# Performance work log

Hardware: AMD Instinct MI355X
Metric: run time of the kernel (lower is better)

Reference implementation:

```python
import jax, jax.numpy as jnp
import numpy as np

DIM = 512
HEADS = 8
DIM_HEAD = 64
INNER = HEADS * DIM_HEAD
SCALE = DIM_HEAD ** -0.5


def setup_inputs() -> dict:
    key = jax.random.key(0)
    ks = jax.random.split(key, 7)
    B, N = 8, 1024
    x = jax.random.normal(ks[0], (B, N, DIM), dtype=jnp.float32)
    rel_pos_bias = jax.random.normal(ks[1], (HEADS, N, N), dtype=jnp.float32) * 0.02
    w_qkv = jax.random.normal(ks[2], (DIM, 3 * INNER), dtype=jnp.float32) * (DIM ** -0.5)
    w_out = jax.random.normal(ks[3], (INNER, DIM), dtype=jnp.float32) * (INNER ** -0.5)
    b_out = jnp.zeros((DIM,), dtype=jnp.float32)
    ln_gamma = jnp.ones((DIM,), dtype=jnp.float32)
    ln_beta = jnp.zeros((DIM,), dtype=jnp.float32)
    return {"x": x, "rel_pos_bias": rel_pos_bias, "w_qkv": w_qkv,
            "w_out": w_out, "b_out": b_out, "ln_gamma": ln_gamma, "ln_beta": ln_beta}


def _layernorm(x, gamma, beta, eps=1e-5):
    mu = jnp.mean(x, axis=-1, keepdims=True)
    var = jnp.var(x, axis=-1, keepdims=True)
    return (x - mu) * jax.lax.rsqrt(var + eps) * gamma + beta


def reference(x, rel_pos_bias, w_qkv, w_out, b_out, ln_gamma, ln_beta):
    B, N, _ = x.shape
    xn = _layernorm(x, ln_gamma, ln_beta)
    qkv = xn @ w_qkv  # [B,N,3*INNER]
    q, k, v = jnp.split(qkv, 3, axis=-1)
    # b n (h d) -> b h n d
    reshape = lambda t: t.reshape(B, N, HEADS, DIM_HEAD).transpose(0, 2, 1, 3)
    q, k, v = reshape(q) * SCALE, reshape(k), reshape(v)
    sim = jnp.einsum('bhid,bhjd->bhij', q, k)
    sim = sim + rel_pos_bias  # broadcast [h,N,N] over batch
    attn = jax.nn.softmax(sim, axis=-1)
    out = jnp.einsum('bhij,bhjd->bhid', attn, v)
    out = out.transpose(0, 2, 1, 3).reshape(B, N, INNER)
    return out @ w_out + b_out
```

## Files before the change

kernel.cpp:

```cpp
#include <hip/hip_runtime.h>
#include <hip/hip_bf16.h>

#define DIM 512
#define HEADS 8
#define DHEAD 64
#define INNER 512
#define NSEQ 1024
#define BATCH 8
#define MROWS (BATCH*NSEQ)
#define QK_SCALE 0.125f

typedef __attribute__((ext_vector_type(4))) float f32x4;
typedef __attribute__((ext_vector_type(8))) short short8;
typedef unsigned short ushort_t;

__device__ inline ushort_t f2bf(float f) {
    __hip_bfloat16 h = __float2bfloat16(f);
    return *reinterpret_cast<ushort_t*>(&h);
}
__device__ inline float bf2f(ushort_t u) {
    union { unsigned int i; float f; } c; c.i = ((unsigned int)u) << 16; return c.f;
}

__global__ __launch_bounds__(256) void ln_kernel(const float* __restrict__ x,
        const float* __restrict__ gamma, const float* __restrict__ beta,
        ushort_t* __restrict__ xn) {
    int row = blockIdx.x * 4 + (threadIdx.x >> 6);
    int lane = threadIdx.x & 63;
    const float4* xr = (const float4*)(x + (size_t)row * DIM);
    float4 a0 = xr[lane];
    float4 a1 = xr[lane + 64];
    float s  = a0.x + a0.y + a0.z + a0.w + a1.x + a1.y + a1.z + a1.w;
    float ss = a0.x*a0.x + a0.y*a0.y + a0.z*a0.z + a0.w*a0.w
             + a1.x*a1.x + a1.y*a1.y + a1.z*a1.z + a1.w*a1.w;
    for (int off = 1; off < 64; off <<= 1) {
        s  += __shfl_xor(s, off);
        ss += __shfl_xor(ss, off);
    }
    float mean = s * (1.0f / DIM);
    float var  = ss * (1.0f / DIM) - mean * mean;
    float inv  = rsqrtf(var + 1e-5f);
    const float4* g4 = (const float4*)gamma;
    const float4* b4 = (const float4*)beta;
    float4 g0 = g4[lane], g1 = g4[lane + 64];
    float4 be0 = b4[lane], be1 = b4[lane + 64];
    ushort4 o0, o1;
    o0.x = f2bf((a0.x - mean) * inv * g0.x + be0.x);
    o0.y = f2bf((a0.y - mean) * inv * g0.y + be0.y);
    o0.z = f2bf((a0.z - mean) * inv * g0.z + be0.z);
    o0.w = f2bf((a0.w - mean) * inv * g0.w + be0.w);
    o1.x = f2bf((a1.x - mean) * inv * g1.x + be1.x);
    o1.y = f2bf((a1.y - mean) * inv * g1.y + be1.y);
    o1.z = f2bf((a1.z - mean) * inv * g1.z + be1.z);
    o1.w = f2bf((a1.w - mean) * inv * g1.w + be1.w);
    ushort4* outr = (ushort4*)(xn + (size_t)row * DIM);
    outr[lane] = o0;
    outr[lane + 64] = o1;
}

__global__ __launch_bounds__(256) void transpose_cast(const float* __restrict__ w,
        ushort_t* __restrict__ wt, int ncols) {
    __shared__ ushort_t T[64][72];
    int n0 = blockIdx.x * 64, k0 = blockIdx.y * 64;
    int t = threadIdx.x;
    int kr = t >> 2;
    int nc = (t & 3) * 16;
    const float4* src = (const float4*)(w + (size_t)(k0 + kr) * ncols + n0 + nc);
    float4 f0 = src[0], f1 = src[1], f2 = src[2], f3 = src[3];
    ushort_t tmp[16];
    tmp[0]=f2bf(f0.x); tmp[1]=f2bf(f0.y); tmp[2]=f2bf(f0.z); tmp[3]=f2bf(f0.w);
    tmp[4]=f2bf(f1.x); tmp[5]=f2bf(f1.y); tmp[6]=f2bf(f1.z); tmp[7]=f2bf(f1.w);
    tmp[8]=f2bf(f2.x); tmp[9]=f2bf(f2.y); tmp[10]=f2bf(f2.z); tmp[11]=f2bf(f2.w);
    tmp[12]=f2bf(f3.x); tmp[13]=f2bf(f3.y); tmp[14]=f2bf(f3.z); tmp[15]=f2bf(f3.w);
    *(uint4*)&T[kr][nc]     = *(uint4*)&tmp[0];
    *(uint4*)&T[kr][nc + 8] = *(uint4*)&tmp[8];
    __syncthreads();
    int nr = t >> 2;
    int kc = (t & 3) * 16;
    ushort_t o[16];
    for (int j = 0; j < 16; j++) o[j] = T[kc + j][nr];
    ushort_t* dst = wt + (size_t)(n0 + nr) * 512 + k0 + kc;
    *(uint4*)(dst)     = *(uint4*)&o[0];
    *(uint4*)(dst + 8) = *(uint4*)&o[8];
}

__global__ __launch_bounds__(256) void bias_cvt(const float* __restrict__ in,
        ushort_t* __restrict__ out) {
    int i = blockIdx.x * 256 + threadIdx.x;
    float4 v = ((const float4*)in)[i];
    ushort4 o;
    o.x = f2bf(v.x); o.y = f2bf(v.y); o.z = f2bf(v.z); o.w = f2bf(v.w);
    ((ushort4*)out)[i] = o;
}

__global__ __launch_bounds__(256) void v_transpose(const ushort_t* __restrict__ vb,
        ushort_t* __restrict__ vt) {
    __shared__ ushort_t T[64][72];
    int bh = blockIdx.y;
    int s0 = blockIdx.x * 64;
    int t = threadIdx.x;
    int row = t >> 2, c = (t & 3) * 16;
    const ushort_t* src = vb + ((size_t)bh * NSEQ + s0 + row) * DHEAD + c;
    *(uint4*)&T[row][c]     = *(const uint4*)(src);
    *(uint4*)&T[row][c + 8] = *(const uint4*)(src + 8);
    __syncthreads();
    int d = t >> 2;
    int sq = (t & 3) * 16;
    ushort_t tmp[16];
    for (int j = 0; j < 16; j++) tmp[j] = T[sq + j][d];
    *(uint4*)(vt + ((size_t)bh * DHEAD + d) * NSEQ + s0 + sq)     = *(uint4*)&tmp[0];
    *(uint4*)(vt + ((size_t)bh * DHEAD + d) * NSEQ + s0 + sq + 8) = *(uint4*)&tmp[8];
}

template<int EPI>
__global__ __launch_bounds__(256) void gemm_kernel(
        const ushort_t* __restrict__ A, const ushort_t* __restrict__ Bt,
        ushort_t* __restrict__ qb, ushort_t* __restrict__ kb, ushort_t* __restrict__ vb,
        float* __restrict__ outp, const float* __restrict__ bvec) {
    __shared__ ushort_t Als[128][72];
    __shared__ ushort_t Bls[128][72];
    int t = threadIdx.x;
    int bm = blockIdx.y, bn = blockIdx.x;
    int lane = t & 63, w = t >> 6, wm = w >> 1, wn = w & 1;
    int l15 = lane & 15, l4 = lane >> 4;
    f32x4 acc[4][4] = {};
    int srow = t >> 1;
    int sc   = (t & 1) * 32;

    for (int kt = 0; kt < DIM / 64; ++kt) {
        __syncthreads();
        {
            const ushort_t* ap = A  + (size_t)(bm*128 + srow) * DIM + kt*64 + sc;
            const ushort_t* bp = Bt + (size_t)(bn*128 + srow) * DIM + kt*64 + sc;
            uint4 a0 = *(const uint4*)(ap);
            uint4 a1 = *(const uint4*)(ap + 8);
            uint4 a2 = *(const uint4*)(ap + 16);
            uint4 a3 = *(const uint4*)(ap + 24);
            uint4 b0 = *(const uint4*)(bp);
            uint4 b1 = *(const uint4*)(bp + 8);
            uint4 b2 = *(const uint4*)(bp + 16);
            uint4 b3 = *(const uint4*)(bp + 24);
            *(uint4*)&Als[srow][sc]      = a0;
            *(uint4*)&Als[srow][sc + 8]  = a1;
            *(uint4*)&Als[srow][sc + 16] = a2;
            *(uint4*)&Als[srow][sc + 24] = a3;
            *(uint4*)&Bls[srow][sc]      = b0;
            *(uint4*)&Bls[srow][sc + 8]  = b1;
            *(uint4*)&Bls[srow][sc + 16] = b2;
            *(uint4*)&Bls[srow][sc + 24] = b3;
        }
        __syncthreads();
        for (int ks = 0; ks < 2; ks++) {
            short8 af[4], bfr[4];
            for (int mi = 0; mi < 4; mi++) af[mi]  = *(const short8*)&Als[wm*64 + mi*16 + l15][ks*32 + l4*8];
            for (int ni = 0; ni < 4; ni++) bfr[ni] = *(const short8*)&Bls[wn*64 + ni*16 + l15][ks*32 + l4*8];
            __builtin_amdgcn_s_setprio(1);
            for (int mi = 0; mi < 4; mi++)
                for (int ni = 0; ni < 4; ni++)
                    acc[mi][ni] = __builtin_amdgcn_mfma_f32_16x16x32_bf16(bfr[ni], af[mi], acc[mi][ni], 0, 0, 0);
            __builtin_amdgcn_s_setprio(0);
        }
    }

    for (int mi = 0; mi < 4; mi++) {
        int r = bm*128 + wm*64 + mi*16 + l15;
        for (int ni = 0; ni < 4; ni++) {
            int c = bn*128 + wn*64 + ni*16 + l4*4;
            f32x4 v = acc[mi][ni];
            if (EPI == 0) {
                int part = c >> 9, cw = c & 511;
                int h = cw >> 6, d = cw & 63;
                int b = r >> 10, i = r & 1023;
                size_t off = (((size_t)(b*HEADS + h)) * NSEQ + i) * DHEAD + d;
                ushort4 o;
                if (part == 0) {
                    o.x = f2bf(v[0] * QK_SCALE); o.y = f2bf(v[1] * QK_SCALE);
                    o.z = f2bf(v[2] * QK_SCALE); o.w = f2bf(v[3] * QK_SCALE);
                    *(ushort4*)(qb + off) = o;
                } else if (part == 1) {
                    o.x = f2bf(v[0]); o.y = f2bf(v[1]); o.z = f2bf(v[2]); o.w = f2bf(v[3]);
                    *(ushort4*)(kb + off) = o;
                } else {
                    o.x = f2bf(v[0]); o.y = f2bf(v[1]); o.z = f2bf(v[2]); o.w = f2bf(v[3]);
                    *(ushort4*)(vb + off) = o;
                }
            } else {
                float4 bv = *(const float4*)(bvec + c);
                float4 o2;
                o2.x = v[0] + bv.x; o2.y = v[1] + bv.y;
                o2.z = v[2] + bv.z; o2.w = v[3] + bv.w;
                *(float4*)(outp + (size_t)r * DIM + c) = o2;
            }
        }
    }
}

__global__ __launch_bounds__(256) void attn_kernel(
        const ushort_t* __restrict__ q, const ushort_t* __restrict__ k,
        const ushort_t* __restrict__ vt, const ushort_t* __restrict__ biasb,
        ushort_t* __restrict__ attno) {
    __shared__ ushort_t Kls[64][72];
    __shared__ ushort_t Vtls[64][72];
    __shared__ ushort_t Pls[4][16][72];
    int t = threadIdx.x, lane = t & 63, w = t >> 6;
    int l15 = lane & 15, l4 = lane >> 4;
    int b = blockIdx.z, h = blockIdx.y, q0 = blockIdx.x * 64;
    size_t bh = (size_t)(b * HEADS + h);
    const ushort_t* qp = q  + (bh * NSEQ + q0 + w*16) * DHEAD;
    const ushort_t* kp = k  + bh * NSEQ * DHEAD;
    const ushort_t* vp = vt + bh * DHEAD * NSEQ;
    int qrow = q0 + w*16 + l15;
    const ushort_t* bp = biasb + ((size_t)h * NSEQ + qrow) * NSEQ;

    short8 bq[2];
    bq[0] = *(const short8*)(qp + l15*DHEAD + l4*8);
    bq[1] = *(const short8*)(qp + l15*DHEAD + l4*8 + 32);

    f32x4 o[4] = {};
    float mrun = -INFINITY, lrun = 0.f;

    int srow = t >> 2, sc = (t & 3) * 16;

    uint4 kreg0, kreg1, vreg0, vreg1;
    {
        const ushort_t* ks0 = kp + (size_t)srow * DHEAD + sc;
        const ushort_t* vs0 = vp + (size_t)srow * NSEQ + sc;
        kreg0 = *(const uint4*)(ks0);
        kreg1 = *(const uint4*)(ks0 + 8);
        vreg0 = *(const uint4*)(vs0);
        vreg1 = *(const uint4*)(vs0 + 8);
    }

    for (int kt = 0; kt < NSEQ / 64; ++kt) {
        __syncthreads();
        *(uint4*)&Kls[srow][sc]      = kreg0;
        *(uint4*)&Kls[srow][sc + 8]  = kreg1;
        *(uint4*)&Vtls[srow][sc]     = vreg0;
        *(uint4*)&Vtls[srow][sc + 8] = vreg1;
        __syncthreads();

        if (kt + 1 < NSEQ / 64) {
            const ushort_t* ksn = kp + (size_t)((kt+1)*64 + srow) * DHEAD + sc;
            const ushort_t* vsn = vp + (size_t)srow * NSEQ + (kt+1)*64 + sc;
            kreg0 = *(const uint4*)(ksn);
            kreg1 = *(const uint4*)(ksn + 8);
            vreg0 = *(const uint4*)(vsn);
            vreg1 = *(const uint4*)(vsn + 8);
        }

        f32x4 s[4];
        __builtin_amdgcn_s_setprio(1);
        for (int ni = 0; ni < 4; ni++) {
            f32x4 z = {};
            short8 ak0 = *(const short8*)&Kls[ni*16 + l15][l4*8];
            short8 ak1 = *(const short8*)&Kls[ni*16 + l15][l4*8 + 32];
            z = __builtin_amdgcn_mfma_f32_16x16x32_bf16(ak0, bq[0], z, 0, 0, 0);
            z = __builtin_amdgcn_mfma_f32_16x16x32_bf16(ak1, bq[1], z, 0, 0, 0);
            s[ni] = z;
        }
        __builtin_amdgcn_s_setprio(0);

        float p[16];
        float mj = -INFINITY;
        for (int ni = 0; ni < 4; ni++) {
            ushort4 b4 = *(const ushort4*)(bp + kt*64 + ni*16 + l4*4);
            float v0 = s[ni][0] + bf2f(b4.x);
            float v1 = s[ni][1] + bf2f(b4.y);
            float v2 = s[ni][2] + bf2f(b4.z);
            float v3 = s[ni][3] + bf2f(b4.w);
            p[ni*4+0] = v0; p[ni*4+1] = v1; p[ni*4+2] = v2; p[ni*4+3] = v3;
            mj = fmaxf(mj, fmaxf(fmaxf(v0, v1), fmaxf(v2, v3)));
        }
        mj = fmaxf(mj, __shfl_xor(mj, 16));
        mj = fmaxf(mj, __shfl_xor(mj, 32));
        if (!__all(mj <= mrun + 8.f)) {
            float mnew = fmaxf(mrun, mj);
            float scl = __expf(mrun - mnew);
            lrun *= scl;
            for (int di = 0; di < 4; di++) o[di] *= scl;
            mrun = mnew;
        }
        float rs = 0.f;
        for (int i = 0; i < 16; i++) {
            p[i] = __expf(p[i] - mrun);
            rs += p[i];
        }
        rs += __shfl_xor(rs, 16);
        rs += __shfl_xor(rs, 32);
        lrun += rs;

        for (int ni = 0; ni < 4; ni++) {
            ushort4 pk;
            pk.x = f2bf(p[ni*4+0]); pk.y = f2bf(p[ni*4+1]);
            pk.z = f2bf(p[ni*4+2]); pk.w = f2bf(p[ni*4+3]);
            *(ushort4*)&Pls[w][l15][ni*16 + l4*4] = pk;
        }

        __builtin_amdgcn_s_setprio(1);
        for (int ks2 = 0; ks2 < 2; ks2++) {
            short8 pb = *(const short8*)&Pls[w][l15][ks2*32 + l4*8];
            for (int di = 0; di < 4; di++) {
                short8 av = *(const short8*)&Vtls[di*16 + l15][ks2*32 + l4*8];
                o[di] = __builtin_amdgcn_mfma_f32_16x16x32_bf16(av, pb, o[di], 0, 0, 0);
            }
        }
        __builtin_amdgcn_s_setprio(0);
    }

    float inv = 1.0f / lrun;
    for (int di = 0; di < 4; di++) {
        ushort4 ov;
        ov.x = f2bf(o[di][0] * inv);
        ov.y = f2bf(o[di][1] * inv);
        ov.z = f2bf(o[di][2] * inv);
        ov.w = f2bf(o[di][3] * inv);
        *(ushort4*)(attno + ((size_t)(b*NSEQ + qrow)) * INNER + h*DHEAD + di*16 + l4*4) = ov;
    }
}

extern "C" void kernel_launch(void* const* d_in, const int* in_sizes, int n_in,
                              void* d_out, int out_size, void* d_ws, size_t ws_size,
                              hipStream_t stream) {
    (void)in_sizes; (void)n_in; (void)out_size; (void)ws_size;
    const float* x      = (const float*)d_in[0];
    const float* bias   = (const float*)d_in[1];
    const float* w_qkv  = (const float*)d_in[2];
    const float* w_out  = (const float*)d_in[3];
    const float* b_out  = (const float*)d_in[4];
    const float* gamma  = (const float*)d_in[5];
    const float* beta   = (const float*)d_in[6];
    float* out = (float*)d_out;

    ushort_t* xn    = (ushort_t*)d_ws;
    ushort_t* wqkvT = xn + (size_t)MROWS * DIM;
    ushort_t* woutT = wqkvT + (size_t)1536 * 512;
    ushort_t* qb    = woutT + (size_t)512 * 512;
    ushort_t* kb    = qb + (size_t)MROWS * INNER;
    ushort_t* vb    = kb + (size_t)MROWS * INNER;
    ushort_t* vt    = vb + (size_t)MROWS * INNER;
    ushort_t* attn  = vt + (size_t)MROWS * INNER;
    ushort_t* biasb = attn + (size_t)MROWS * INNER;

    hipLaunchKernelGGL(ln_kernel, dim3(MROWS / 4), dim3(256), 0, stream, x, gamma, beta, xn);
    hipLaunchKernelGGL(transpose_cast, dim3(1536 / 64, 512 / 64), dim3(256), 0, stream, w_qkv, wqkvT, 3 * INNER);
    hipLaunchKernelGGL(transpose_cast, dim3(512 / 64, 512 / 64), dim3(256), 0, stream, w_out, woutT, DIM);
    hipLaunchKernelGGL(bias_cvt, dim3(HEADS * NSEQ * NSEQ / 4 / 256), dim3(256), 0, stream, bias, biasb);
    hipLaunchKernelGGL((gemm_kernel<0>), dim3(1536 / 128, MROWS / 128), dim3(256), 0, stream,
                       xn, wqkvT, qb, kb, vb, nullptr, nullptr);
    hipLaunchKernelGGL(v_transpose, dim3(NSEQ / 64, BATCH * HEADS), dim3(256), 0, stream, vb, vt);
    hipLaunchKernelGGL(attn_kernel, dim3(NSEQ / 64, HEADS, BATCH), dim3(256), 0, stream,
                       qb, kb, vt, biasb, attn);
    hipLaunchKernelGGL((gemm_kernel<1>), dim3(DIM / 128, MROWS / 128), dim3(256), 0, stream,
                       attn, woutT, nullptr, nullptr, nullptr, out, b_out);
}
```

Measured before the change: 203.8 us.

## Fuse prep kernels, write V transposed, prefetch GEMM tiles, use exp2 softmax

Merges layernorm, both weight transpose-casts and the bias conversion into one prep kernel. The QKV GEMM epilogue now writes V directly in transposed layout, which removes the separate v_transpose kernel. Both GEMMs gain register prefetch of the next K tile, and the output GEMM uses a 64-wide N tile so more blocks launch. In the attention kernel, log2e is folded into Q and the bias so the softmax can use raw v_exp_f32, and the next bias tile is prefetched into registers. The transposed V stores are scalar and strided, which may cost write efficiency.

```diff
diff --git a/kernel.cpp b/kernel.cpp
--- a/kernel.cpp
+++ b/kernel.cpp
@@ -9,6 +9,7 @@
 #define BATCH 8
 #define MROWS (BATCH*NSEQ)
 #define QK_SCALE 0.125f
+#define LOG2E 1.44269504f
 
 typedef __attribute__((ext_vector_type(4))) float f32x4;
 typedef __attribute__((ext_vector_type(8))) short short8;
@@ -21,48 +22,12 @@
 __device__ inline float bf2f(ushort_t u) {
     union { unsigned int i; float f; } c; c.i = ((unsigned int)u) << 16; return c.f;
 }
-
-__global__ __launch_bounds__(256) void ln_kernel(const float* __restrict__ x,
-        const float* __restrict__ gamma, const float* __restrict__ beta,
-        ushort_t* __restrict__ xn) {
-    int row = blockIdx.x * 4 + (threadIdx.x >> 6);
-    int lane = threadIdx.x & 63;
-    const float4* xr = (const float4*)(x + (size_t)row * DIM);
-    float4 a0 = xr[lane];
-    float4 a1 = xr[lane + 64];
-    float s  = a0.x + a0.y + a0.z + a0.w + a1.x + a1.y + a1.z + a1.w;
-    float ss = a0.x*a0.x + a0.y*a0.y + a0.z*a0.z + a0.w*a0.w
-             + a1.x*a1.x + a1.y*a1.y + a1.z*a1.z + a1.w*a1.w;
-    for (int off = 1; off < 64; off <<= 1) {
-        s  += __shfl_xor(s, off);
-        ss += __shfl_xor(ss, off);
-    }
-    float mean = s * (1.0f / DIM);
-    float var  = ss * (1.0f / DIM) - mean * mean;
-    float inv  = rsqrtf(var + 1e-5f);
-    const float4* g4 = (const float4*)gamma;
-    const float4* b4 = (const float4*)beta;
-    float4 g0 = g4[lane], g1 = g4[lane + 64];
-    float4 be0 = b4[lane], be1 = b4[lane + 64];
-    ushort4 o0, o1;
-    o0.x = f2bf((a0.x - mean) * inv * g0.x + be0.x);
-    o0.y = f2bf((a0.y - mean) * inv * g0.y + be0.y);
-    o0.z = f2bf((a0.z - mean) * inv * g0.z + be0.z);
-    o0.w = f2bf((a0.w - mean) * inv * g0.w + be0.w);
-    o1.x = f2bf((a1.x - mean) * inv * g1.x + be1.x);
-    o1.y = f2bf((a1.y - mean) * inv * g1.y + be1.y);
-    o1.z = f2bf((a1.z - mean) * inv * g1.z + be1.z);
-    o1.w = f2bf((a1.w - mean) * inv * g1.w + be1.w);
-    ushort4* outr = (ushort4*)(xn + (size_t)row * DIM);
-    outr[lane] = o0;
-    outr[lane + 64] = o1;
-}
-
-__global__ __launch_bounds__(256) void transpose_cast(const float* __restrict__ w,
-        ushort_t* __restrict__ wt, int ncols) {
-    __shared__ ushort_t T[64][72];
-    int n0 = blockIdx.x * 64, k0 = blockIdx.y * 64;
-    int t = threadIdx.x;
+__device__ inline float fast_exp2(float x) {
+    float r; asm("v_exp_f32 %0, %1" : "=v"(r) : "v"(x)); return r;
+}
+
+__device__ inline void tc_tile(const float* __restrict__ w, ushort_t* __restrict__ wt,
+        int ncols, int n0, int k0, int t, ushort_t (*T)[72]) {
     int kr = t >> 2;
     int nc = (t & 3) * 16;
     const float4* src = (const float4*)(w + (size_t)(k0 + kr) * ncols + n0 + nc);
@@ -84,79 +49,109 @@
     *(uint4*)(dst + 8) = *(uint4*)&o[8];
 }
 
-__global__ __launch_bounds__(256) void bias_cvt(const float* __restrict__ in,
-        ushort_t* __restrict__ out) {
-    int i = blockIdx.x * 256 + threadIdx.x;
-    float4 v = ((const float4*)in)[i];
-    ushort4 o;
-    o.x = f2bf(v.x); o.y = f2bf(v.y); o.z = f2bf(v.z); o.w = f2bf(v.w);
-    ((ushort4*)out)[i] = o;
-}
-
-__global__ __launch_bounds__(256) void v_transpose(const ushort_t* __restrict__ vb,
-        ushort_t* __restrict__ vt) {
+__global__ __launch_bounds__(256) void prep_kernel(
+        const float* __restrict__ x, const float* __restrict__ gamma,
+        const float* __restrict__ beta, ushort_t* __restrict__ xn,
+        const float* __restrict__ w_qkv, ushort_t* __restrict__ wqkvT,
+        const float* __restrict__ w_out, ushort_t* __restrict__ woutT,
+        const float* __restrict__ bias, ushort_t* __restrict__ biasb) {
     __shared__ ushort_t T[64][72];
-    int bh = blockIdx.y;
-    int s0 = blockIdx.x * 64;
+    int bid = blockIdx.x;
     int t = threadIdx.x;
-    int row = t >> 2, c = (t & 3) * 16;
-    const ushort_t* src = vb + ((size_t)bh * NSEQ + s0 + row) * DHEAD + c;
-    *(uint4*)&T[row][c]     = *(const uint4*)(src);
-    *(uint4*)&T[row][c + 8] = *(const uint4*)(src + 8);
-    __syncthreads();
-    int d = t >> 2;
-    int sq = (t & 3) * 16;
-    ushort_t tmp[16];
-    for (int j = 0; j < 16; j++) tmp[j] = T[sq + j][d];
-    *(uint4*)(vt + ((size_t)bh * DHEAD + d) * NSEQ + s0 + sq)     = *(uint4*)&tmp[0];
-    *(uint4*)(vt + ((size_t)bh * DHEAD + d) * NSEQ + s0 + sq + 8) = *(uint4*)&tmp[8];
-}
-
-template<int EPI>
+    if (bid < 2048) {
+        int row = bid * 4 + (t >> 6);
+        int lane = t & 63;
+        const float4* xr = (const float4*)(x + (size_t)row * DIM);
+        float4 a0 = xr[lane];
+        float4 a1 = xr[lane + 64];
+        float s  = a0.x + a0.y + a0.z + a0.w + a1.x + a1.y + a1.z + a1.w;
+        float ss = a0.x*a0.x + a0.y*a0.y + a0.z*a0.z + a0.w*a0.w
+                 + a1.x*a1.x + a1.y*a1.y + a1.z*a1.z + a1.w*a1.w;
+        for (int off = 1; off < 64; off <<= 1) {
+            s  += __shfl_xor(s, off);
+            ss += __shfl_xor(ss, off);
+        }
+        float mean = s * (1.0f / DIM);
+        float var  = ss * (1.0f / DIM) - mean * mean;
+        float inv  = rsqrtf(var + 1e-5f);
+        const float4* g4 = (const float4*)gamma;
+        const float4* b4 = (const float4*)beta;
+        float4 g0 = g4[lane], g1 = g4[lane + 64];
+        float4 be0 = b4[lane], be1 = b4[lane + 64];
+        ushort4 o0, o1;
+        o0.x = f2bf((a0.x - mean) * inv * g0.x + be0.x);
+        o0.y = f2bf((a0.y - mean) * inv * g0.y + be0.y);
+        o0.z = f2bf((a0.z - mean) * inv * g0.z + be0.z);
+        o0.w = f2bf((a0.w - mean) * inv * g0.w + be0.w);
+        o1.x = f2bf((a1.x - mean) * inv * g1.x + be1.x);
+        o1.y = f2bf((a1.y - mean) * inv * g1.y + be1.y);
+        o1.z = f2bf((a1.z - mean) * inv * g1.z + be1.z);
+        o1.w = f2bf((a1.w - mean) * inv * g1.w + be1.w);
+        ushort4* outr = (ushort4*)(xn + (size_t)row * DIM);
+        outr[lane] = o0;
+        outr[lane + 64] = o1;
+    } else if (bid < 2240) {
+        int rel = bid - 2048;
+        tc_tile(w_qkv, wqkvT, 1536, (rel % 24) * 64, (rel / 24) * 64, t, T);
+    } else if (bid < 2304) {
+        int rel = bid - 2240;
+        tc_tile(w_out, woutT, 512, (rel % 8) * 64, (rel / 8) * 64, t, T);
+    } else {
+        int rel = bid - 2304;
+        int i = rel * 256 + t;
+        float4 v = ((const float4*)bias)[i];
+        ushort4 o;
+        o.x = f2bf(v.x * LOG2E); o.y = f2bf(v.y * LOG2E);
+        o.z = f2bf(v.z * LOG2E); o.w = f2bf(v.w * LOG2E);
+        ((ushort4*)biasb)[i] = o;
+    }
+}
+
+template<int EPI, int BN>
 __global__ __launch_bounds__(256) void gemm_kernel(
         const ushort_t* __restrict__ A, const ushort_t* __restrict__ Bt,
-        ushort_t* __restrict__ qb, ushort_t* __restrict__ kb, ushort_t* __restrict__ vb,
+        ushort_t* __restrict__ qb, ushort_t* __restrict__ kb, ushort_t* __restrict__ vtb,
         float* __restrict__ outp, const float* __restrict__ bvec) {
+    constexpr int BNF = BN / 32;
     __shared__ ushort_t Als[128][72];
-    __shared__ ushort_t Bls[128][72];
+    __shared__ ushort_t Bls[BN][72];
     int t = threadIdx.x;
     int bm = blockIdx.y, bn = blockIdx.x;
     int lane = t & 63, w = t >> 6, wm = w >> 1, wn = w & 1;
     int l15 = lane & 15, l4 = lane >> 4;
-    f32x4 acc[4][4] = {};
-    int srow = t >> 1;
-    int sc   = (t & 1) * 32;
+    f32x4 acc[4][BNF] = {};
+
+    int ra = t >> 1, ca = (t & 1) * 32;
+    int rb, cb_;
+    if constexpr (BN == 128) { rb = t >> 1; cb_ = (t & 1) * 32; }
+    else                     { rb = t >> 2; cb_ = (t & 3) * 16; }
+
+    uint4 ar[4], br[BN == 128 ? 4 : 2];
+    {
+        const ushort_t* ap = A  + (size_t)(bm*128 + ra) * DIM + ca;
+        for (int i = 0; i < 4; i++) ar[i] = *(const uint4*)(ap + i*8);
+        const ushort_t* bp = Bt + (size_t)(bn*BN + rb) * DIM + cb_;
+        for (int i = 0; i < (BN == 128 ? 4 : 2); i++) br[i] = *(const uint4*)(bp + i*8);
+    }
 
     for (int kt = 0; kt < DIM / 64; ++kt) {
         __syncthreads();
-        {
-            const ushort_t* ap = A  + (size_t)(bm*128 + srow) * DIM + kt*64 + sc;
-            const ushort_t* bp = Bt + (size_t)(bn*128 + srow) * DIM + kt*64 + sc;
-            uint4 a0 = *(const uint4*)(ap);
-            uint4 a1 = *(const uint4*)(ap + 8);
-            uint4 a2 = *(const uint4*)(ap + 16);
-            uint4 a3 = *(const uint4*)(ap + 24);
-            uint4 b0 = *(const uint4*)(bp);
-            uint4 b1 = *(const uint4*)(bp + 8);
-            uint4 b2 = *(const uint4*)(bp + 16);
-            uint4 b3 = *(const uint4*)(bp + 24);
-            *(uint4*)&Als[srow][sc]      = a0;
-            *(uint4*)&Als[srow][sc + 8]  = a1;
-            *(uint4*)&Als[srow][sc + 16] = a2;
-            *(uint4*)&Als[srow][sc + 24] = a3;
-            *(uint4*)&Bls[srow][sc]      = b0;
-            *(uint4*)&Bls[srow][sc + 8]  = b1;
-            *(uint4*)&Bls[srow][sc + 16] = b2;
-            *(uint4*)&Bls[srow][sc + 24] = b3;
-        }
+        for (int i = 0; i < 4; i++) *(uint4*)&Als[ra][ca + i*8] = ar[i];
+        for (int i = 0; i < (BN == 128 ? 4 : 2); i++) *(uint4*)&Bls[rb][cb_ + i*8] = br[i];
         __syncthreads();
+        if (kt + 1 < DIM / 64) {
+            const ushort_t* ap = A  + (size_t)(bm*128 + ra) * DIM + (kt+1)*64 + ca;
+            for (int i = 0; i < 4; i++) ar[i] = *(const uint4*)(ap + i*8);
+            const ushort_t* bp = Bt + (size_t)(bn*BN + rb) * DIM + (kt+1)*64 + cb_;
+            for (int i = 0; i < (BN == 128 ? 4 : 2); i++) br[i] = *(const uint4*)(bp + i*8);
+        }
         for (int ks = 0; ks < 2; ks++) {
-            short8 af[4], bfr[4];
-            for (int mi = 0; mi < 4; mi++) af[mi]  = *(const short8*)&Als[wm*64 + mi*16 + l15][ks*32 + l4*8];
-            for (int ni = 0; ni < 4; ni++) bfr[ni] = *(const short8*)&Bls[wn*64 + ni*16 + l15][ks*32 + l4*8];
+            short8 af[4], bfr[BNF];
+            for (int mi = 0; mi < 4; mi++)   af[mi]  = *(const short8*)&Als[wm*64 + mi*16 + l15][ks*32 + l4*8];
+            for (int ni = 0; ni < BNF; ni++) bfr[ni] = *(const short8*)&Bls[wn*(BN/2) + ni*16 + l15][ks*32 + l4*8];
             __builtin_amdgcn_s_setprio(1);
             for (int mi = 0; mi < 4; mi++)
-                for (int ni = 0; ni < 4; ni++)
+                for (int ni = 0; ni < BNF; ni++)
                     acc[mi][ni] = __builtin_amdgcn_mfma_f32_16x16x32_bf16(bfr[ni], af[mi], acc[mi][ni], 0, 0, 0);
             __builtin_amdgcn_s_setprio(0);
         }
@@ -164,25 +159,26 @@
 
     for (int mi = 0; mi < 4; mi++) {
         int r = bm*128 + wm*64 + mi*16 + l15;
-        for (int ni = 0; ni < 4; ni++) {
-            int c = bn*128 + wn*64 + ni*16 + l4*4;
+        for (int ni = 0; ni < BNF; ni++) {
+            int c = bn*BN + wn*(BN/2) + ni*16 + l4*4;
             f32x4 v = acc[mi][ni];
             if (EPI == 0) {
                 int part = c >> 9, cw = c & 511;
                 int h = cw >> 6, d = cw & 63;
                 int b = r >> 10, i = r & 1023;
-                size_t off = (((size_t)(b*HEADS + h)) * NSEQ + i) * DHEAD + d;
-                ushort4 o;
+                size_t bh = (size_t)(b*HEADS + h);
                 if (part == 0) {
-                    o.x = f2bf(v[0] * QK_SCALE); o.y = f2bf(v[1] * QK_SCALE);
-                    o.z = f2bf(v[2] * QK_SCALE); o.w = f2bf(v[3] * QK_SCALE);
-                    *(ushort4*)(qb + off) = o;
+                    ushort4 o;
+                    o.x = f2bf(v[0] * (QK_SCALE*LOG2E)); o.y = f2bf(v[1] * (QK_SCALE*LOG2E));
+                    o.z = f2bf(v[2] * (QK_SCALE*LOG2E)); o.w = f2bf(v[3] * (QK_SCALE*LOG2E));
+                    *(ushort4*)(qb + (bh * NSEQ + i) * DHEAD + d) = o;
                 } else if (part == 1) {
+                    ushort4 o;
                     o.x = f2bf(v[0]); o.y = f2bf(v[1]); o.z = f2bf(v[2]); o.w = f2bf(v[3]);
-                    *(ushort4*)(kb + off) = o;
+                    *(ushort4*)(kb + (bh * NSEQ + i) * DHEAD + d) = o;
                 } else {
-                    o.x = f2bf(v[0]); o.y = f2bf(v[1]); o.z = f2bf(v[2]); o.w = f2bf(v[3]);
-                    *(ushort4*)(vb + off) = o;
+                    for (int j = 0; j < 4; j++)
+                        vtb[(bh * DHEAD + d + j) * NSEQ + i] = f2bf(v[j]);
                 }
             } else {
                 float4 bv = *(const float4*)(bvec + c);
@@ -222,6 +218,7 @@
     int srow = t >> 2, sc = (t & 3) * 16;
 
     uint4 kreg0, kreg1, vreg0, vreg1;
+    ushort4 cb[4], nb[4];
     {
         const ushort_t* ks0 = kp + (size_t)srow * DHEAD + sc;
         const ushort_t* vs0 = vp + (size_t)srow * NSEQ + sc;
@@ -229,6 +226,8 @@
         kreg1 = *(const uint4*)(ks0 + 8);
         vreg0 = *(const uint4*)(vs0);
         vreg1 = *(const uint4*)(vs0 + 8);
+        for (int ni = 0; ni < 4; ni++)
+            cb[ni] = *(const ushort4*)(bp + ni*16 + l4*4);
     }
 
     for (int kt = 0; kt < NSEQ / 64; ++kt) {
@@ -263,7 +262,7 @@
         float p[16];
         float mj = -INFINITY;
         for (int ni = 0; ni < 4; ni++) {
-            ushort4 b4 = *(const ushort4*)(bp + kt*64 + ni*16 + l4*4);
+            ushort4 b4 = cb[ni];
             float v0 = s[ni][0] + bf2f(b4.x);
             float v1 = s[ni][1] + bf2f(b4.y);
             float v2 = s[ni][2] + bf2f(b4.z);
@@ -273,16 +272,20 @@
         }
         mj = fmaxf(mj, __shfl_xor(mj, 16));
         mj = fmaxf(mj, __shfl_xor(mj, 32));
+        if (kt + 1 < NSEQ / 64) {
+            for (int ni = 0; ni < 4; ni++)
+                nb[ni] = *(const ushort4*)(bp + (kt+1)*64 + ni*16 + l4*4);
+        }
         if (!__all(mj <= mrun + 8.f)) {
             float mnew = fmaxf(mrun, mj);
-            float scl = __expf(mrun - mnew);
+            float scl = fast_exp2(mrun - mnew);
             lrun *= scl;
             for (int di = 0; di < 4; di++) o[di] *= scl;
             mrun = mnew;
         }
         float rs = 0.f;
         for (int i = 0; i < 16; i++) {
-            p[i] = __expf(p[i] - mrun);
+            p[i] = fast_exp2(p[i] - mrun);
             rs += p[i];
         }
         rs += __shfl_xor(rs, 16);
@@ -305,6 +308,8 @@
             }
         }
         __builtin_amdgcn_s_setprio(0);
+
+        for (int ni = 0; ni < 4; ni++) cb[ni] = nb[ni];
     }
 
     float inv = 1.0f / lrun;
@@ -336,20 +341,16 @@
     ushort_t* woutT = wqkvT + (size_t)1536 * 512;
     ushort_t* qb    = woutT + (size_t)512 * 512;
     ushort_t* kb    = qb + (size_t)MROWS * INNER;
-    ushort_t* vb    = kb + (size_t)MROWS * INNER;
-    ushort_t* vt    = vb + (size_t)MROWS * INNER;
+    ushort_t* vt    = kb + (size_t)MROWS * INNER;
     ushort_t* attn  = vt + (size_t)MROWS * INNER;
     ushort_t* biasb = attn + (size_t)MROWS * INNER;
 
-    hipLaunchKernelGGL(ln_kernel, dim3(MROWS / 4), dim3(256), 0, stream, x, gamma, beta, xn);
-    hipLaunchKernelGGL(transpose_cast, dim3(1536 / 64, 512 / 64), dim3(256), 0, stream, w_qkv, wqkvT, 3 * INNER);
-    hipLaunchKernelGGL(transpose_cast, dim3(512 / 64, 512 / 64), dim3(256), 0, stream, w_out, woutT, DIM);
-    hipLaunchKernelGGL(bias_cvt, dim3(HEADS * NSEQ * NSEQ / 4 / 256), dim3(256), 0, stream, bias, biasb);
-    hipLaunchKernelGGL((gemm_kernel<0>), dim3(1536 / 128, MROWS / 128), dim3(256), 0, stream,
-                       xn, wqkvT, qb, kb, vb, nullptr, nullptr);
-    hipLaunchKernelGGL(v_transpose, dim3(NSEQ / 64, BATCH * HEADS), dim3(256), 0, stream, vb, vt);
+    hipLaunchKernelGGL(prep_kernel, dim3(10496), dim3(256), 0, stream,
+                       x, gamma, beta, xn, w_qkv, wqkvT, w_out, woutT, bias, biasb);
+    hipLaunchKernelGGL((gemm_kernel<0, 128>), dim3(1536 / 128, MROWS / 128), dim3(256), 0, stream,
+                       xn, wqkvT, qb, kb, vt, nullptr, nullptr);
     hipLaunchKernelGGL(attn_kernel, dim3(NSEQ / 64, HEADS, BATCH), dim3(256), 0, stream,
                        qb, kb, vt, biasb, attn);
-    hipLaunchKernelGGL((gemm_kernel<1>), dim3(DIM / 128, MROWS / 128), dim3(256), 0, stream,
+    hipLaunchKernelGGL((gemm_kernel<1, 64>), dim3(DIM / 64, MROWS / 128), dim3(256), 0, stream,
                        attn, woutT, nullptr, nullptr, nullptr, out, b_out);
 }
```

Measured after the change: 250.3 us. +22.8%, slower.
